# Performance work log

Measured on AMD Instinct MI355X. Metric: run time of the kernel, lower is better.

Reference implementation:

```python
import jax, jax.numpy as jnp
import numpy as np

N = 8192
IN_CH = 256
HID = 256
NEG_INF = -1000000000.0


def setup_inputs() -> dict:
    key = jax.random.key(0)
    ks = jax.random.split(key, 7)
    inlayer = jax.random.normal(ks[0], (N, IN_CH), dtype=jnp.float32)
    adj_mat = jax.random.randint(ks[1], (N, N), 0, 2, dtype=jnp.int32)
    # Xavier-uniform style scales
    s0 = (6.0 / (IN_CH + HID)) ** 0.5
    s1 = (6.0 / (HID + 1)) ** 0.5
    W = jax.random.uniform(ks[2], (HID, IN_CH), jnp.float32, -s0, s0)   # conv1d.weight[:, :, 0]
    w1 = jax.random.uniform(ks[3], (1, HID), jnp.float32, -s1, s1)      # conv1d1.weight[:, :, 0]
    b1 = jax.random.uniform(ks[4], (1,), jnp.float32, -s1, s1)          # conv1d1.bias
    w2 = jax.random.uniform(ks[5], (1, HID), jnp.float32, -s1, s1)      # conv1d2.weight[:, :, 0]
    b2 = jax.random.uniform(ks[6], (1,), jnp.float32, -s1, s1)          # conv1d2.bias
    return {"inlayer": inlayer, "adj_mat": adj_mat, "W": W,
            "w1": w1, "b1": b1, "w2": w2, "b2": b2}


def reference(inlayer, adj_mat, W, w1, b1, w2, b2):
    # 1x1 conv == linear projection: in_fts [HID, N]
    in_fts = W @ inlayer.T
    f1 = (w1 @ in_fts).T + b1          # [N, 1]
    f2 = (w2 @ in_fts).T + b2          # [N, 1]
    logits = f1 + f2.T                 # [N, N] broadcast add
    bias_mat = jnp.where(adj_mat > 0, 0.0, NEG_INF).astype(logits.dtype)
    coefs = jax.nn.softmax(jax.nn.leaky_relu(logits) + bias_mat, axis=-1)
    vals = coefs @ inlayer             # [N, IN_CH]
    return vals
```

## Files before the change

kernel.cpp:

```cpp
#include <hip/hip_runtime.h>
#include <hip/hip_bf16.h>

typedef float f32x4 __attribute__((ext_vector_type(4)));
typedef __bf16 bf16x8 __attribute__((ext_vector_type(8)));

#define N 8192
#define CH 256
#define NJC 2
#define JCW (N / NJC)
#define JT 128
#define NT (JCW / JT)
#define BM 64

static constexpr size_t OFF_P1 = 0;
static constexpr size_t OFF_P2 = 32768;
static constexpr size_t OFF_T1 = 65536;
static constexpr size_t OFF_T2 = 66560;
static constexpr size_t OFF_F1 = 67584;
static constexpr size_t OFF_F2 = OFF_F1 + (size_t)N * 4;
static constexpr size_t OFF_XT = 262144;
static constexpr size_t OFF_SP = OFF_XT + (size_t)CH * N * 2;
static constexpr size_t OFF_PV = OFF_SP + (size_t)NJC * N * 4;

__global__ __launch_bounds__(256) void k1a(
    const float* __restrict__ W, const float* __restrict__ w1,
    const float* __restrict__ w2, float* __restrict__ p1, float* __restrict__ p2)
{
    int b = blockIdx.x, c = threadIdx.x;
    float a1 = 0.f, a2 = 0.f;
#pragma unroll
    for (int hh = 0; hh < 8; ++hh) {
        int h = b * 8 + hh;
        float wv = W[h * CH + c];
        a1 = __builtin_fmaf(w1[h], wv, a1);
        a2 = __builtin_fmaf(w2[h], wv, a2);
    }
    p1[b * CH + c] = a1;
    p2[b * CH + c] = a2;
}

__global__ __launch_bounds__(256) void k1b(
    const float* __restrict__ p1, const float* __restrict__ p2,
    float* __restrict__ t1, float* __restrict__ t2)
{
    int c = threadIdx.x;
    float a1 = 0.f, a2 = 0.f;
#pragma unroll 8
    for (int b = 0; b < 32; ++b) { a1 += p1[b * CH + c]; a2 += p2[b * CH + c]; }
    t1[c] = a1;
    t2[c] = a2;
}

__global__ __launch_bounds__(256) void ktf(
    const float* __restrict__ x, const float* __restrict__ t1,
    const float* __restrict__ t2, const float* __restrict__ b1,
    const float* __restrict__ b2, unsigned short* __restrict__ xtp,
    float* __restrict__ f1, float* __restrict__ f2)
{
    __shared__ unsigned short tile[32][264];
    int js32 = blockIdx.x;
    int jb = js32 * 32;
    int t = threadIdx.x;
    int lane = t & 63;
    int wv = t >> 6;
    const float4* t1v = (const float4*)t1;
    const float4* t2v = (const float4*)t2;
    float4 ta = t1v[lane], tb = t2v[lane];
    float bb1 = b1[0], bb2 = b2[0];
#pragma unroll
    for (int it = 0; it < 8; ++it) {
        int jr = it * 4 + wv;
        float4 v = *(const float4*)(x + (size_t)(jb + jr) * CH + lane * 4);
        __hip_bfloat16 h0 = __float2bfloat16(v.x);
        __hip_bfloat16 h1 = __float2bfloat16(v.y);
        __hip_bfloat16 h2 = __float2bfloat16(v.z);
        __hip_bfloat16 h3 = __float2bfloat16(v.w);
        tile[jr][lane * 4 + 0] = *(unsigned short*)&h0;
        tile[jr][lane * 4 + 1] = *(unsigned short*)&h1;
        tile[jr][lane * 4 + 2] = *(unsigned short*)&h2;
        tile[jr][lane * 4 + 3] = *(unsigned short*)&h3;
        float d1 = v.x * ta.x + v.y * ta.y + v.z * ta.z + v.w * ta.w;
        float d2 = v.x * tb.x + v.y * tb.y + v.z * tb.z + v.w * tb.w;
#pragma unroll
        for (int off = 32; off; off >>= 1) {
            d1 += __shfl_down(d1, off);
            d2 += __shfl_down(d2, off);
        }
        if (lane == 0) { f1[jb + jr] = d1 + bb1; f2[jb + jr] = d2 + bb2; }
    }
    __syncthreads();
    int r = lane & 15, q = lane >> 4;
#pragma unroll
    for (int pass = 0; pass < 4; ++pass) {
        int ct = pass * 4 + wv;
        unsigned short vs[8];
#pragma unroll
        for (int e = 0; e < 8; ++e) vs[e] = tile[q * 8 + e][ct * 16 + r];
        size_t u = ((size_t)ct * 256 + js32) * 64 + lane;
        *(ulonglong2*)(xtp + u * 8) = *(ulonglong2*)vs;
    }
}

#define BAR() { asm volatile("s_waitcnt lgkmcnt(0)" ::: "memory"); \
                __builtin_amdgcn_s_barrier(); }

__global__ __launch_bounds__(1024, 4) void k34_fused(
    const int* __restrict__ adj, const float* __restrict__ f1,
    const float* __restrict__ f2, const unsigned short* __restrict__ xtp,
    float* __restrict__ pv0, float* __restrict__ pvx, float* __restrict__ s_part)
{
    __shared__ __align__(16) unsigned short P[2][BM * JT];
    __shared__ __align__(16) float f2s[JCW];

    const int tid = threadIdx.x;
    const int lane = tid & 63;
    const int w = tid >> 6;
    const int r = lane & 15, q = lane >> 4;
    const int bid = blockIdx.x;
    const int jc = bid & 1;
    const int rb = (bid >> 1) * BM;
    const int jbase = jc * JCW;
    const bool cons = (w < 8);

    const int ptid = tid - 512;
    const int prow = (ptid >> 3) & 63;
    const int pjo = (ptid & 7) * 16;
    const int* aptr = adj + (size_t)(rb + prow) * N + jbase + pjo;
    const int s0i = (ptid & 7) * 2;
    const int wu0 = prow * 16 + (s0i ^ (prow & 7));
    const int wu1 = prow * 16 + ((s0i + 1) ^ (prow & 7));
    float f1r = 0.f;
    if (!cons) f1r = f1[rb + prow];

    const unsigned short* xb0 = xtp + (((size_t)(w * 2) * 256 + jc * (JCW / 32)) * 64 + lane) * 8;
    const unsigned short* xb1 = xtp + (((size_t)(w * 2 + 1) * 256 + jc * (JCW / 32)) * 64 + lane) * 8;

    f32x4 acc[4][2];
#pragma unroll
    for (int mt = 0; mt < 4; ++mt)
#pragma unroll
        for (int nt = 0; nt < 2; ++nt) acc[mt][nt] = (f32x4){0.f, 0.f, 0.f, 0.f};
    float s_acc = 0.f;

    int4 RA0, RA1, RA2, RA3, RB0, RB1, RB2, RB3;

#define LOAD_A(R0, R1, R2, R3, t)                                   \
    { const int4* p_ = (const int4*)(aptr + (size_t)(t) * JT);      \
      R0 = p_[0]; R1 = p_[1]; R2 = p_[2]; R3 = p_[3]; }
#define EXPW(R0, R1, R2, R3, buf, tt)                               \
    { float4 g0 = *(const float4*)(&f2s[(tt) * JT + pjo]);          \
      float4 g1 = *(const float4*)(&f2s[(tt) * JT + pjo + 4]);      \
      float4 g2 = *(const float4*)(&f2s[(tt) * JT + pjo + 8]);      \
      float4 g3 = *(const float4*)(&f2s[(tt) * JT + pjo + 12]);     \
      int av[16] = {R0.x, R0.y, R0.z, R0.w, R1.x, R1.y, R1.z, R1.w, \
                    R2.x, R2.y, R2.z, R2.w, R3.x, R3.y, R3.z, R3.w};\
      float gv[16] = {g0.x, g0.y, g0.z, g0.w, g1.x, g1.y, g1.z, g1.w,\
                      g2.x, g2.y, g2.z, g2.w, g3.x, g3.y, g3.z, g3.w};\
      bf16x8 pk0, pk1;                                              \
      _Pragma("unroll")                                             \
      for (int e = 0; e < 16; ++e) {                                \
          float t_ = f1r + gv[e];                                   \
          t_ = fmaxf(t_, 0.01f * t_);                               \
          float p_ = (av[e] > 0) ? __expf(t_) : 0.f;                \
          s_acc += p_;                                              \
          if (e < 8) pk0[e] = (__bf16)p_; else pk1[e - 8] = (__bf16)p_; \
      }                                                             \
      *reinterpret_cast<bf16x8*>(&P[buf][(size_t)wu0 * 8]) = pk0;   \
      *reinterpret_cast<bf16x8*>(&P[buf][(size_t)wu1 * 8]) = pk1; }
#define MFMA_TILE(tt, buf)                                          \
    { _Pragma("unroll")                                             \
      for (int kk = 0; kk < 4; ++kk) {                              \
          bf16x8 B0 = *(const bf16x8*)(xb0 + ((size_t)((tt) * 4 + kk) * 64) * 8); \
          bf16x8 B1 = *(const bf16x8*)(xb1 + ((size_t)((tt) * 4 + kk) * 64) * 8); \
          _Pragma("unroll")                                         \
          for (int mt = 0; mt < 4; ++mt) {                          \
              int u_ = (mt * 16 + r) * 16 + ((kk * 4 + q) ^ (r & 7)); \
              bf16x8 A = *(const bf16x8*)(&P[buf][(size_t)u_ * 8]); \
              acc[mt][0] = __builtin_amdgcn_mfma_f32_16x16x32_bf16(A, B0, acc[mt][0], 0, 0, 0); \
              acc[mt][1] = __builtin_amdgcn_mfma_f32_16x16x32_bf16(A, B1, acc[mt][1], 0, 0, 0); \
          }                                                         \
      } }

    *(float4*)(&f2s[tid * 4]) = *(const float4*)(f2 + jbase + tid * 4);

    if (!cons) {
        LOAD_A(RA0, RA1, RA2, RA3, 0);
        LOAD_A(RB0, RB1, RB2, RB3, 1);
    }
    __syncthreads();
    if (!cons) EXPW(RA0, RA1, RA2, RA3, 0, 0);
    BAR();

    for (int t = 0; t < NT; t += 2) {
        if (cons) {
            MFMA_TILE(t, 0);
        } else {
            if (t + 2 < NT) LOAD_A(RA0, RA1, RA2, RA3, t + 2);
            EXPW(RB0, RB1, RB2, RB3, 1, t + 1);
        }
        BAR();
        if (cons) {
            MFMA_TILE(t + 1, 1);
        } else {
            if (t + 3 < NT) LOAD_A(RB0, RB1, RB2, RB3, t + 3);
            if (t + 2 < NT) EXPW(RA0, RA1, RA2, RA3, 0, t + 2);
        }
        BAR();
    }

    if (!cons) {
        s_acc += __shfl_xor(s_acc, 1);
        s_acc += __shfl_xor(s_acc, 2);
        s_acc += __shfl_xor(s_acc, 4);
        if ((lane & 7) == 0) s_part[jc * N + rb + prow] = s_acc;
    } else {
        float* dst = (jc == 0) ? pv0 : pvx;
#pragma unroll
        for (int mt = 0; mt < 4; ++mt)
#pragma unroll
            for (int nt = 0; nt < 2; ++nt)
#pragma unroll
                for (int reg = 0; reg < 4; ++reg) {
                    int row = rb + mt * 16 + q * 4 + reg;
                    int col = w * 32 + nt * 16 + r;
                    dst[(size_t)row * CH + col] = acc[mt][nt][reg];
                }
    }
#undef LOAD_A
#undef EXPW
#undef MFMA_TILE
}

__global__ __launch_bounds__(256) void k5_reduce(
    const float* __restrict__ pvx, const float* __restrict__ s_part,
    float* __restrict__ out)
{
    int g = blockIdx.x * 256 + threadIdx.x;
    int row = g >> 6;
    float s = s_part[row] + s_part[N + row];
    float inv = (s != 0.f) ? 1.0f / s : 0.f;
    float4* out4 = (float4*)out;
    const float4* p1 = (const float4*)pvx;
    float4 v = out4[g];
    float4 a = p1[g];
    v.x = (v.x + a.x) * inv;
    v.y = (v.y + a.y) * inv;
    v.z = (v.z + a.z) * inv;
    v.w = (v.w + a.w) * inv;
    out4[g] = v;
}

extern "C" void kernel_launch(void* const* d_in, const int* in_sizes, int n_in,
                              void* d_out, int out_size, void* d_ws, size_t ws_size,
                              hipStream_t stream)
{
    const float* inlayer = (const float*)d_in[0];
    const int*   adj     = (const int*)d_in[1];
    const float* W       = (const float*)d_in[2];
    const float* w1      = (const float*)d_in[3];
    const float* b1      = (const float*)d_in[4];
    const float* w2      = (const float*)d_in[5];
    const float* b2      = (const float*)d_in[6];
    float* out = (float*)d_out;

    char* ws = (char*)d_ws;
    float* p1 = (float*)(ws + OFF_P1);
    float* p2 = (float*)(ws + OFF_P2);
    float* t1 = (float*)(ws + OFF_T1);
    float* t2 = (float*)(ws + OFF_T2);
    float* f1 = (float*)(ws + OFF_F1);
    float* f2 = (float*)(ws + OFF_F2);
    unsigned short* xtp = (unsigned short*)(ws + OFF_XT);
    float* s_part = (float*)(ws + OFF_SP);
    float* pvx = (float*)(ws + OFF_PV);

    k1a<<<dim3(32), dim3(256), 0, stream>>>(W, w1, w2, p1, p2);
    k1b<<<dim3(1), dim3(256), 0, stream>>>(p1, p2, t1, t2);
    ktf<<<dim3(N / 32), dim3(256), 0, stream>>>(
        inlayer, t1, t2, b1, b2, xtp, f1, f2);
    k34_fused<<<dim3((N / BM) * NJC), dim3(1024), 0, stream>>>(
        adj, f1, f2, xtp, out, pvx, s_part);
    k5_reduce<<<dim3(N * CH / 4 / 256), dim3(256), 0, stream>>>(pvx, s_part, out);
}
```

Measured before the change: 101.8 us.

## Split columns into four chunks with 512-thread blocks and wider per-wave MFMA tiles

Moves the fused attention kernel from a 2-way to a 4-way split of the key dimension and halves the j-tile width. Blocks shrink to 512 threads (4 consumer and 4 producer waves). Each consumer wave now covers 64 output columns with 4x4 accumulators, and its MFMA section is raised in priority with s_setprio. This gives twice as many smaller blocks to improve occupancy and load balance, at the cost of two extra partial-output buffers that the reduce kernel must read and sum.

```diff
diff --git a/kernel.cpp b/kernel.cpp
--- a/kernel.cpp
+++ b/kernel.cpp
@@ -6,9 +6,9 @@
 
 #define N 8192
 #define CH 256
-#define NJC 2
+#define NJC 4
 #define JCW (N / NJC)
-#define JT 128
+#define JT 64
 #define NT (JCW / JT)
 #define BM 64
 
@@ -104,7 +104,7 @@
 #define BAR() { asm volatile("s_waitcnt lgkmcnt(0)" ::: "memory"); \
                 __builtin_amdgcn_s_barrier(); }
 
-__global__ __launch_bounds__(1024, 4) void k34_fused(
+__global__ __launch_bounds__(512, 4) void k34_fused(
     const int* __restrict__ adj, const float* __restrict__ f1,
     const float* __restrict__ f2, const unsigned short* __restrict__ xtp,
     float* __restrict__ pv0, float* __restrict__ pvx, float* __restrict__ s_part)
@@ -117,29 +117,26 @@
     const int w = tid >> 6;
     const int r = lane & 15, q = lane >> 4;
     const int bid = blockIdx.x;
-    const int jc = bid & 1;
-    const int rb = (bid >> 1) * BM;
+    const int jc = bid & 3;
+    const int rb = (bid >> 2) * BM;
     const int jbase = jc * JCW;
-    const bool cons = (w < 8);
-
-    const int ptid = tid - 512;
-    const int prow = (ptid >> 3) & 63;
-    const int pjo = (ptid & 7) * 16;
+    const bool cons = (w < 4);
+
+    const int ptid = (tid - 256) & 255;
+    const int prow = ptid >> 2;
+    const int pjo = (ptid & 3) * 16;
     const int* aptr = adj + (size_t)(rb + prow) * N + jbase + pjo;
-    const int s0i = (ptid & 7) * 2;
-    const int wu0 = prow * 16 + (s0i ^ (prow & 7));
-    const int wu1 = prow * 16 + ((s0i + 1) ^ (prow & 7));
+    const int s0i = (ptid & 3) * 2;
+    const int wu0 = prow * 8 + (s0i ^ (prow & 7));
+    const int wu1 = prow * 8 + ((s0i + 1) ^ (prow & 7));
     float f1r = 0.f;
     if (!cons) f1r = f1[rb + prow];
 
-    const unsigned short* xb0 = xtp + (((size_t)(w * 2) * 256 + jc * (JCW / 32)) * 64 + lane) * 8;
-    const unsigned short* xb1 = xtp + (((size_t)(w * 2 + 1) * 256 + jc * (JCW / 32)) * 64 + lane) * 8;
-
-    f32x4 acc[4][2];
+    f32x4 acc[4][4];
 #pragma unroll
     for (int mt = 0; mt < 4; ++mt)
 #pragma unroll
-        for (int nt = 0; nt < 2; ++nt) acc[mt][nt] = (f32x4){0.f, 0.f, 0.f, 0.f};
+        for (int i = 0; i < 4; ++i) acc[mt][i] = (f32x4){0.f, 0.f, 0.f, 0.f};
     float s_acc = 0.f;
 
     int4 RA0, RA1, RA2, RA3, RB0, RB1, RB2, RB3;
@@ -168,25 +165,31 @@
       *reinterpret_cast<bf16x8*>(&P[buf][(size_t)wu0 * 8]) = pk0;   \
       *reinterpret_cast<bf16x8*>(&P[buf][(size_t)wu1 * 8]) = pk1; }
 #define MFMA_TILE(tt, buf)                                          \
-    { _Pragma("unroll")                                             \
-      for (int kk = 0; kk < 4; ++kk) {                              \
-          bf16x8 B0 = *(const bf16x8*)(xb0 + ((size_t)((tt) * 4 + kk) * 64) * 8); \
-          bf16x8 B1 = *(const bf16x8*)(xb1 + ((size_t)((tt) * 4 + kk) * 64) * 8); \
+    { __builtin_amdgcn_s_setprio(1);                                \
+      _Pragma("unroll")                                             \
+      for (int kk = 0; kk < 2; ++kk) {                              \
+          bf16x8 Bv[4];                                             \
+          _Pragma("unroll")                                         \
+          for (int i = 0; i < 4; ++i) {                             \
+              size_t u_ = ((size_t)(w * 4 + i) * 256 + jc * 64 + (tt) * 2 + kk) * 64 + lane; \
+              Bv[i] = *(const bf16x8*)(xtp + u_ * 8);               \
+          }                                                         \
           _Pragma("unroll")                                         \
           for (int mt = 0; mt < 4; ++mt) {                          \
-              int u_ = (mt * 16 + r) * 16 + ((kk * 4 + q) ^ (r & 7)); \
-              bf16x8 A = *(const bf16x8*)(&P[buf][(size_t)u_ * 8]); \
-              acc[mt][0] = __builtin_amdgcn_mfma_f32_16x16x32_bf16(A, B0, acc[mt][0], 0, 0, 0); \
-              acc[mt][1] = __builtin_amdgcn_mfma_f32_16x16x32_bf16(A, B1, acc[mt][1], 0, 0, 0); \
+              int ua = (mt * 16 + r) * 8 + ((kk * 4 + q) ^ (r & 7));\
+              bf16x8 A = *(const bf16x8*)(&P[buf][(size_t)ua * 8]); \
+              _Pragma("unroll")                                     \
+              for (int i = 0; i < 4; ++i)                           \
+                  acc[mt][i] = __builtin_amdgcn_mfma_f32_16x16x32_bf16(A, Bv[i], acc[mt][i], 0, 0, 0); \
           }                                                         \
-      } }
-
-    *(float4*)(&f2s[tid * 4]) = *(const float4*)(f2 + jbase + tid * 4);
+      }                                                             \
+      __builtin_amdgcn_s_setprio(0); }
 
     if (!cons) {
         LOAD_A(RA0, RA1, RA2, RA3, 0);
         LOAD_A(RB0, RB1, RB2, RB3, 1);
     }
+    *(float4*)(&f2s[tid * 4]) = *(const float4*)(f2 + jbase + tid * 4);
     __syncthreads();
     if (!cons) EXPW(RA0, RA1, RA2, RA3, 0, 0);
     BAR();
@@ -211,19 +214,18 @@
     if (!cons) {
         s_acc += __shfl_xor(s_acc, 1);
         s_acc += __shfl_xor(s_acc, 2);
-        s_acc += __shfl_xor(s_acc, 4);
-        if ((lane & 7) == 0) s_part[jc * N + rb + prow] = s_acc;
+        if ((lane & 3) == 0) s_part[jc * N + rb + prow] = s_acc;
     } else {
-        float* dst = (jc == 0) ? pv0 : pvx;
+        float* dst = (jc == 0) ? pv0 : (pvx + (size_t)(jc - 1) * N * CH);
 #pragma unroll
         for (int mt = 0; mt < 4; ++mt)
 #pragma unroll
-            for (int nt = 0; nt < 2; ++nt)
+            for (int i = 0; i < 4; ++i)
 #pragma unroll
                 for (int reg = 0; reg < 4; ++reg) {
                     int row = rb + mt * 16 + q * 4 + reg;
-                    int col = w * 32 + nt * 16 + r;
-                    dst[(size_t)row * CH + col] = acc[mt][nt][reg];
+                    int col = (w * 4 + i) * 16 + r;
+                    dst[(size_t)row * CH + col] = acc[mt][i][reg];
                 }
     }
 #undef LOAD_A
@@ -237,16 +239,18 @@
 {
     int g = blockIdx.x * 256 + threadIdx.x;
     int row = g >> 6;
-    float s = s_part[row] + s_part[N + row];
+    float s = s_part[row] + s_part[N + row] + s_part[2 * N + row] + s_part[3 * N + row];
     float inv = (s != 0.f) ? 1.0f / s : 0.f;
     float4* out4 = (float4*)out;
     const float4* p1 = (const float4*)pvx;
+    const float4* p2 = p1 + (size_t)N * CH / 4;
+    const float4* p3 = p2 + (size_t)N * CH / 4;
     float4 v = out4[g];
-    float4 a = p1[g];
-    v.x = (v.x + a.x) * inv;
-    v.y = (v.y + a.y) * inv;
-    v.z = (v.z + a.z) * inv;
-    v.w = (v.w + a.w) * inv;
+    float4 a = p1[g], b = p2[g], c = p3[g];
+    v.x = (v.x + a.x + b.x + c.x) * inv;
+    v.y = (v.y + a.y + b.y + c.y) * inv;
+    v.z = (v.z + a.z + b.z + c.z) * inv;
+    v.w = (v.w + a.w + b.w + c.w) * inv;
     out4[g] = v;
 }
 
@@ -278,7 +282,7 @@
     k1b<<<dim3(1), dim3(256), 0, stream>>>(p1, p2, t1, t2);
     ktf<<<dim3(N / 32), dim3(256), 0, stream>>>(
         inlayer, t1, t2, b1, b2, xtp, f1, f2);
-    k34_fused<<<dim3((N / BM) * NJC), dim3(1024), 0, stream>>>(
+    k34_fused<<<dim3((N / BM) * NJC), dim3(512), 0, stream>>>(
         adj, f1, f2, xtp, out, pvx, s_part);
     k5_reduce<<<dim3(N * CH / 4 / 256), dim3(256), 0, stream>>>(pvx, s_part, out);
 }
```

After: 162.4 us. +59.6%, slower.

## Replace producer/consumer LDS pipeline with register-resident per-wave exp+MFMA over 8 column splits

Applied to the files above, without the earlier changes.

The attention kernel drops the warp-specialized producer/consumer scheme that staged bf16 probabilities through shared memory with barriers. Each wave now computes exp weights for 32 rows directly into MFMA A-operand registers and multiplies them against the pre-packed bf16 features loaded straight from global memory, accumulating all 256 output columns in registers. The column dimension is split 8 ways instead of 2 to keep enough blocks in flight, so the reduce kernel now sums 8 partial outputs and 8 partial row sums. This removes LDS traffic and barriers but raises register pressure, re-reads the feature matrix per wave from L2, and adds extra partial-output write and read traffic.

```diff
diff --git a/kernel.cpp b/kernel.cpp
--- a/kernel.cpp
+++ b/kernel.cpp
@@ -6,11 +6,9 @@
 
 #define N 8192
 #define CH 256
-#define NJC 2
+#define NJC 8
 #define JCW (N / NJC)
-#define JT 128
-#define NT (JCW / JT)
-#define BM 64
+#define NS (JCW / 32)
 
 static constexpr size_t OFF_P1 = 0;
 static constexpr size_t OFF_P2 = 32768;
@@ -101,134 +99,97 @@
     }
 }
 
-#define BAR() { asm volatile("s_waitcnt lgkmcnt(0)" ::: "memory"); \
-                __builtin_amdgcn_s_barrier(); }
-
-__global__ __launch_bounds__(1024, 4) void k34_fused(
+__global__ __launch_bounds__(256, 2) void k34_fused(
     const int* __restrict__ adj, const float* __restrict__ f1,
     const float* __restrict__ f2, const unsigned short* __restrict__ xtp,
     float* __restrict__ pv0, float* __restrict__ pvx, float* __restrict__ s_part)
 {
-    __shared__ __align__(16) unsigned short P[2][BM * JT];
-    __shared__ __align__(16) float f2s[JCW];
-
     const int tid = threadIdx.x;
     const int lane = tid & 63;
     const int w = tid >> 6;
     const int r = lane & 15, q = lane >> 4;
     const int bid = blockIdx.x;
-    const int jc = bid & 1;
-    const int rb = (bid >> 1) * BM;
+    const int jc = bid & 7;
+    const int rb = (bid >> 3) * 128 + w * 32;
     const int jbase = jc * JCW;
-    const bool cons = (w < 8);
-
-    const int ptid = tid - 512;
-    const int prow = (ptid >> 3) & 63;
-    const int pjo = (ptid & 7) * 16;
-    const int* aptr = adj + (size_t)(rb + prow) * N + jbase + pjo;
-    const int s0i = (ptid & 7) * 2;
-    const int wu0 = prow * 16 + (s0i ^ (prow & 7));
-    const int wu1 = prow * 16 + ((s0i + 1) ^ (prow & 7));
-    float f1r = 0.f;
-    if (!cons) f1r = f1[rb + prow];
-
-    const unsigned short* xb0 = xtp + (((size_t)(w * 2) * 256 + jc * (JCW / 32)) * 64 + lane) * 8;
-    const unsigned short* xb1 = xtp + (((size_t)(w * 2 + 1) * 256 + jc * (JCW / 32)) * 64 + lane) * 8;
-
-    f32x4 acc[4][2];
-#pragma unroll
-    for (int mt = 0; mt < 4; ++mt)
-#pragma unroll
-        for (int nt = 0; nt < 2; ++nt) acc[mt][nt] = (f32x4){0.f, 0.f, 0.f, 0.f};
-    float s_acc = 0.f;
-
-    int4 RA0, RA1, RA2, RA3, RB0, RB1, RB2, RB3;
-
-#define LOAD_A(R0, R1, R2, R3, t)                                   \
-    { const int4* p_ = (const int4*)(aptr + (size_t)(t) * JT);      \
-      R0 = p_[0]; R1 = p_[1]; R2 = p_[2]; R3 = p_[3]; }
-#define EXPW(R0, R1, R2, R3, buf, tt)                               \
-    { float4 g0 = *(const float4*)(&f2s[(tt) * JT + pjo]);          \
-      float4 g1 = *(const float4*)(&f2s[(tt) * JT + pjo + 4]);      \
-      float4 g2 = *(const float4*)(&f2s[(tt) * JT + pjo + 8]);      \
-      float4 g3 = *(const float4*)(&f2s[(tt) * JT + pjo + 12]);     \
-      int av[16] = {R0.x, R0.y, R0.z, R0.w, R1.x, R1.y, R1.z, R1.w, \
-                    R2.x, R2.y, R2.z, R2.w, R3.x, R3.y, R3.z, R3.w};\
-      float gv[16] = {g0.x, g0.y, g0.z, g0.w, g1.x, g1.y, g1.z, g1.w,\
-                      g2.x, g2.y, g2.z, g2.w, g3.x, g3.y, g3.z, g3.w};\
-      bf16x8 pk0, pk1;                                              \
+
+    const float f1r0 = f1[rb + r];
+    const float f1r1 = f1[rb + 16 + r];
+    const int* arow0 = adj + (size_t)(rb + r) * N + jbase + q * 8;
+    const int* arow1 = arow0 + (size_t)16 * N;
+    const float* f2p = f2 + jbase + q * 8;
+
+    f32x4 acc0[16], acc1[16];
+#pragma unroll
+    for (int ct = 0; ct < 16; ++ct) {
+        acc0[ct] = (f32x4){0.f, 0.f, 0.f, 0.f};
+        acc1[ct] = (f32x4){0.f, 0.f, 0.f, 0.f};
+    }
+    float s0 = 0.f, s1 = 0.f;
+
+    int4 A0a, A0b, A1a, A1b;
+    int4 B0a, B0b, B1a, B1b;
+
+#define LOAD(Xa, Xb, Ya, Yb, t)                                     \
+    { const int4* p0_ = (const int4*)(arow0 + (size_t)(t) * 32);    \
+      const int4* p1_ = (const int4*)(arow1 + (size_t)(t) * 32);    \
+      Xa = p0_[0]; Xb = p0_[1]; Ya = p1_[0]; Yb = p1_[1]; }
+#define COMPUTE(Xa, Xb, Ya, Yb, t)                                  \
+    { float4 g0 = *(const float4*)(f2p + (size_t)(t) * 32);         \
+      float4 g1 = *(const float4*)(f2p + (size_t)(t) * 32 + 4);     \
+      int av0[8] = {Xa.x, Xa.y, Xa.z, Xa.w, Xb.x, Xb.y, Xb.z, Xb.w};\
+      int av1[8] = {Ya.x, Ya.y, Ya.z, Ya.w, Yb.x, Yb.y, Yb.z, Yb.w};\
+      float gv[8] = {g0.x, g0.y, g0.z, g0.w, g1.x, g1.y, g1.z, g1.w};\
+      bf16x8 pka, pkb;                                              \
       _Pragma("unroll")                                             \
-      for (int e = 0; e < 16; ++e) {                                \
-          float t_ = f1r + gv[e];                                   \
-          t_ = fmaxf(t_, 0.01f * t_);                               \
-          float p_ = (av[e] > 0) ? __expf(t_) : 0.f;                \
-          s_acc += p_;                                              \
-          if (e < 8) pk0[e] = (__bf16)p_; else pk1[e - 8] = (__bf16)p_; \
+      for (int e = 0; e < 8; ++e) {                                 \
+          float ta_ = f1r0 + gv[e];                                 \
+          ta_ = fmaxf(ta_, 0.01f * ta_);                            \
+          float pa_ = (av0[e] > 0) ? __expf(ta_) : 0.f;             \
+          s0 += pa_;                                                \
+          pka[e] = (__bf16)pa_;                                     \
+          float tb_ = f1r1 + gv[e];                                 \
+          tb_ = fmaxf(tb_, 0.01f * tb_);                            \
+          float pb_ = (av1[e] > 0) ? __expf(tb_) : 0.f;             \
+          s1 += pb_;                                                \
+          pkb[e] = (__bf16)pb_;                                     \
       }                                                             \
-      *reinterpret_cast<bf16x8*>(&P[buf][(size_t)wu0 * 8]) = pk0;   \
-      *reinterpret_cast<bf16x8*>(&P[buf][(size_t)wu1 * 8]) = pk1; }
-#define MFMA_TILE(tt, buf)                                          \
-    { _Pragma("unroll")                                             \
-      for (int kk = 0; kk < 4; ++kk) {                              \
-          bf16x8 B0 = *(const bf16x8*)(xb0 + ((size_t)((tt) * 4 + kk) * 64) * 8); \
-          bf16x8 B1 = *(const bf16x8*)(xb1 + ((size_t)((tt) * 4 + kk) * 64) * 8); \
-          _Pragma("unroll")                                         \
-          for (int mt = 0; mt < 4; ++mt) {                          \
-              int u_ = (mt * 16 + r) * 16 + ((kk * 4 + q) ^ (r & 7)); \
-              bf16x8 A = *(const bf16x8*)(&P[buf][(size_t)u_ * 8]); \
-              acc[mt][0] = __builtin_amdgcn_mfma_f32_16x16x32_bf16(A, B0, acc[mt][0], 0, 0, 0); \
-              acc[mt][1] = __builtin_amdgcn_mfma_f32_16x16x32_bf16(A, B1, acc[mt][1], 0, 0, 0); \
-          }                                                         \
+      _Pragma("unroll")                                             \
+      for (int ct = 0; ct < 16; ++ct) {                             \
+          size_t u_ = ((size_t)ct * 256 + jc * NS + (t)) * 64 + lane; \
+          bf16x8 Bv = *(const bf16x8*)(xtp + u_ * 8);               \
+          acc0[ct] = __builtin_amdgcn_mfma_f32_16x16x32_bf16(pka, Bv, acc0[ct], 0, 0, 0); \
+          acc1[ct] = __builtin_amdgcn_mfma_f32_16x16x32_bf16(pkb, Bv, acc1[ct], 0, 0, 0); \
       } }
 
-    *(float4*)(&f2s[tid * 4]) = *(const float4*)(f2 + jbase + tid * 4);
-
-    if (!cons) {
-        LOAD_A(RA0, RA1, RA2, RA3, 0);
-        LOAD_A(RB0, RB1, RB2, RB3, 1);
-    }
-    __syncthreads();
-    if (!cons) EXPW(RA0, RA1, RA2, RA3, 0, 0);
-    BAR();
-
-    for (int t = 0; t < NT; t += 2) {
-        if (cons) {
-            MFMA_TILE(t, 0);
-        } else {
-            if (t + 2 < NT) LOAD_A(RA0, RA1, RA2, RA3, t + 2);
-            EXPW(RB0, RB1, RB2, RB3, 1, t + 1);
+    LOAD(A0a, A0b, A1a, A1b, 0);
+    LOAD(B0a, B0b, B1a, B1b, 1);
+
+    for (int t = 0; t < NS; t += 2) {
+        COMPUTE(A0a, A0b, A1a, A1b, t);
+        if (t + 2 < NS) LOAD(A0a, A0b, A1a, A1b, t + 2);
+        COMPUTE(B0a, B0b, B1a, B1b, t + 1);
+        if (t + 3 < NS) LOAD(B0a, B0b, B1a, B1b, t + 3);
+    }
+
+    s0 += __shfl_xor(s0, 16); s0 += __shfl_xor(s0, 32);
+    s1 += __shfl_xor(s1, 16); s1 += __shfl_xor(s1, 32);
+    if (lane < 16) {
+        s_part[(size_t)jc * N + rb + lane] = s0;
+        s_part[(size_t)jc * N + rb + 16 + lane] = s1;
+    }
+
+    float* dst = (jc == 0) ? pv0 : (pvx + (size_t)(jc - 1) * N * CH);
+#pragma unroll
+    for (int ct = 0; ct < 16; ++ct)
+#pragma unroll
+        for (int reg = 0; reg < 4; ++reg) {
+            int row0 = rb + q * 4 + reg;
+            dst[(size_t)row0 * CH + ct * 16 + r] = acc0[ct][reg];
+            dst[(size_t)(row0 + 16) * CH + ct * 16 + r] = acc1[ct][reg];
         }
-        BAR();
-        if (cons) {
-            MFMA_TILE(t + 1, 1);
-        } else {
-            if (t + 3 < NT) LOAD_A(RB0, RB1, RB2, RB3, t + 3);
-            if (t + 2 < NT) EXPW(RA0, RA1, RA2, RA3, 0, t + 2);
-        }
-        BAR();
-    }
-
-    if (!cons) {
-        s_acc += __shfl_xor(s_acc, 1);
-        s_acc += __shfl_xor(s_acc, 2);
-        s_acc += __shfl_xor(s_acc, 4);
-        if ((lane & 7) == 0) s_part[jc * N + rb + prow] = s_acc;
-    } else {
-        float* dst = (jc == 0) ? pv0 : pvx;
-#pragma unroll
-        for (int mt = 0; mt < 4; ++mt)
-#pragma unroll
-            for (int nt = 0; nt < 2; ++nt)
-#pragma unroll
-                for (int reg = 0; reg < 4; ++reg) {
-                    int row = rb + mt * 16 + q * 4 + reg;
-                    int col = w * 32 + nt * 16 + r;
-                    dst[(size_t)row * CH + col] = acc[mt][nt][reg];
-                }
-    }
-#undef LOAD_A
-#undef EXPW
-#undef MFMA_TILE
+#undef LOAD
+#undef COMPUTE
 }
 
 __global__ __launch_bounds__(256) void k5_reduce(
@@ -237,16 +198,18 @@
 {
     int g = blockIdx.x * 256 + threadIdx.x;
     int row = g >> 6;
-    float s = s_part[row] + s_part[N + row];
+    float s = 0.f;
+#pragma unroll
+    for (int k = 0; k < NJC; ++k) s += s_part[(size_t)k * N + row];
     float inv = (s != 0.f) ? 1.0f / s : 0.f;
     float4* out4 = (float4*)out;
-    const float4* p1 = (const float4*)pvx;
     float4 v = out4[g];
-    float4 a = p1[g];
-    v.x = (v.x + a.x) * inv;
-    v.y = (v.y + a.y) * inv;
-    v.z = (v.z + a.z) * inv;
-    v.w = (v.w + a.w) * inv;
+#pragma unroll
+    for (int k = 0; k < NJC - 1; ++k) {
+        float4 a = ((const float4*)(pvx + (size_t)k * N * CH))[g];
+        v.x += a.x; v.y += a.y; v.z += a.z; v.w += a.w;
+    }
+    v.x *= inv; v.y *= inv; v.z *= inv; v.w *= inv;
     out4[g] = v;
 }
 
@@ -278,7 +241,7 @@
     k1b<<<dim3(1), dim3(256), 0, stream>>>(p1, p2, t1, t2);
     ktf<<<dim3(N / 32), dim3(256), 0, stream>>>(
         inlayer, t1, t2, b1, b2, xtp, f1, f2);
-    k34_fused<<<dim3((N / BM) * NJC), dim3(1024), 0, stream>>>(
+    k34_fused<<<dim3((N / 128) * NJC), dim3(256), 0, stream>>>(
         adj, f1, f2, xtp, out, pvx, s_part);
     k5_reduce<<<dim3(N * CH / 4 / 256), dim3(256), 0, stream>>>(pvx, s_part, out);
 }
```

Result: slower. 176.1 us (+73.0%).

## Factor exp of leaky-relu into precomputed per-node exponentials and split columns four ways

Applied to the files above, without the earlier changes.

Replaces the per-element exp(leaky_relu(f1+f2)) with a product of exponentials precomputed per node: exp(f1)*exp(f2) when the logit is positive, otherwise exp(0.01 f1)*exp(0.01 f2). The hot loop then does multiplies and a select instead of a transcendental. The column split also goes from 2 to 4 chunks with a higher occupancy hint, and the final reduction sums more partials. The risk is that products of large exponentials overflow in fp32, since there is no max subtraction. It also adds more partial-output traffic and LDS per block.

```diff
diff --git a/kernel.cpp b/kernel.cpp
--- a/kernel.cpp
+++ b/kernel.cpp
@@ -6,7 +6,7 @@
 
 #define N 8192
 #define CH 256
-#define NJC 2
+#define NJC 4
 #define JCW (N / NJC)
 #define JT 128
 #define NT (JCW / JT)
@@ -16,8 +16,10 @@
 static constexpr size_t OFF_P2 = 32768;
 static constexpr size_t OFF_T1 = 65536;
 static constexpr size_t OFF_T2 = 66560;
-static constexpr size_t OFF_F1 = 67584;
-static constexpr size_t OFF_F2 = OFF_F1 + (size_t)N * 4;
+static constexpr size_t OFF_E1 = 67584;
+static constexpr size_t OFF_G1 = OFF_E1 + (size_t)N * 4;
+static constexpr size_t OFF_E2 = OFF_G1 + (size_t)N * 4;
+static constexpr size_t OFF_G2 = OFF_E2 + (size_t)N * 4;
 static constexpr size_t OFF_XT = 262144;
 static constexpr size_t OFF_SP = OFF_XT + (size_t)CH * N * 2;
 static constexpr size_t OFF_PV = OFF_SP + (size_t)NJC * N * 4;
@@ -55,7 +57,8 @@
     const float* __restrict__ x, const float* __restrict__ t1,
     const float* __restrict__ t2, const float* __restrict__ b1,
     const float* __restrict__ b2, unsigned short* __restrict__ xtp,
-    float* __restrict__ f1, float* __restrict__ f2)
+    float* __restrict__ E1g, float* __restrict__ G1g,
+    float* __restrict__ E2g, float* __restrict__ G2g)
 {
     __shared__ unsigned short tile[32][264];
     int js32 = blockIdx.x;
@@ -86,7 +89,13 @@
             d1 += __shfl_down(d1, off);
             d2 += __shfl_down(d2, off);
         }
-        if (lane == 0) { f1[jb + jr] = d1 + bb1; f2[jb + jr] = d2 + bb2; }
+        if (lane == 0) {
+            float f1 = d1 + bb1, f2 = d2 + bb2;
+            E1g[jb + jr] = __expf(f1);
+            G1g[jb + jr] = __expf(0.01f * f1);
+            E2g[jb + jr] = __expf(f2);
+            G2g[jb + jr] = __expf(0.01f * f2);
+        }
     }
     __syncthreads();
     int r = lane & 15, q = lane >> 4;
@@ -104,21 +113,23 @@
 #define BAR() { asm volatile("s_waitcnt lgkmcnt(0)" ::: "memory"); \
                 __builtin_amdgcn_s_barrier(); }
 
-__global__ __launch_bounds__(1024, 4) void k34_fused(
-    const int* __restrict__ adj, const float* __restrict__ f1,
-    const float* __restrict__ f2, const unsigned short* __restrict__ xtp,
+__global__ __launch_bounds__(1024, 8) void k34_fused(
+    const int* __restrict__ adj, const float* __restrict__ E1g,
+    const float* __restrict__ G1g, const float* __restrict__ E2g,
+    const float* __restrict__ G2g, const unsigned short* __restrict__ xtp,
     float* __restrict__ pv0, float* __restrict__ pvx, float* __restrict__ s_part)
 {
     __shared__ __align__(16) unsigned short P[2][BM * JT];
-    __shared__ __align__(16) float f2s[JCW];
+    __shared__ __align__(16) float e2s[JCW];
+    __shared__ __align__(16) float g2s[JCW];
 
     const int tid = threadIdx.x;
     const int lane = tid & 63;
     const int w = tid >> 6;
     const int r = lane & 15, q = lane >> 4;
     const int bid = blockIdx.x;
-    const int jc = bid & 1;
-    const int rb = (bid >> 1) * BM;
+    const int jc = bid & 3;
+    const int rb = (bid >> 2) * BM;
     const int jbase = jc * JCW;
     const bool cons = (w < 8);
 
@@ -129,8 +140,8 @@
     const int s0i = (ptid & 7) * 2;
     const int wu0 = prow * 16 + (s0i ^ (prow & 7));
     const int wu1 = prow * 16 + ((s0i + 1) ^ (prow & 7));
-    float f1r = 0.f;
-    if (!cons) f1r = f1[rb + prow];
+    float E1r = 0.f, G1r = 0.f;
+    if (!cons) { E1r = E1g[rb + prow]; G1r = G1g[rb + prow]; }
 
     const unsigned short* xb0 = xtp + (((size_t)(w * 2) * 256 + jc * (JCW / 32)) * 64 + lane) * 8;
     const unsigned short* xb1 = xtp + (((size_t)(w * 2 + 1) * 256 + jc * (JCW / 32)) * 64 + lane) * 8;
@@ -148,20 +159,27 @@
     { const int4* p_ = (const int4*)(aptr + (size_t)(t) * JT);      \
       R0 = p_[0]; R1 = p_[1]; R2 = p_[2]; R3 = p_[3]; }
 #define EXPW(R0, R1, R2, R3, buf, tt)                               \
-    { float4 g0 = *(const float4*)(&f2s[(tt) * JT + pjo]);          \
-      float4 g1 = *(const float4*)(&f2s[(tt) * JT + pjo + 4]);      \
-      float4 g2 = *(const float4*)(&f2s[(tt) * JT + pjo + 8]);      \
-      float4 g3 = *(const float4*)(&f2s[(tt) * JT + pjo + 12]);     \
+    { float4 g0 = *(const float4*)(&e2s[(tt) * JT + pjo]);          \
+      float4 g1 = *(const float4*)(&e2s[(tt) * JT + pjo + 4]);      \
+      float4 g2 = *(const float4*)(&e2s[(tt) * JT + pjo + 8]);      \
+      float4 g3 = *(const float4*)(&e2s[(tt) * JT + pjo + 12]);     \
+      float4 h0 = *(const float4*)(&g2s[(tt) * JT + pjo]);          \
+      float4 h1 = *(const float4*)(&g2s[(tt) * JT + pjo + 4]);      \
+      float4 h2 = *(const float4*)(&g2s[(tt) * JT + pjo + 8]);      \
+      float4 h3 = *(const float4*)(&g2s[(tt) * JT + pjo + 12]);     \
       int av[16] = {R0.x, R0.y, R0.z, R0.w, R1.x, R1.y, R1.z, R1.w, \
                     R2.x, R2.y, R2.z, R2.w, R3.x, R3.y, R3.z, R3.w};\
       float gv[16] = {g0.x, g0.y, g0.z, g0.w, g1.x, g1.y, g1.z, g1.w,\
                       g2.x, g2.y, g2.z, g2.w, g3.x, g3.y, g3.z, g3.w};\
+      float hv[16] = {h0.x, h0.y, h0.z, h0.w, h1.x, h1.y, h1.z, h1.w,\
+                      h2.x, h2.y, h2.z, h2.w, h3.x, h3.y, h3.z, h3.w};\
       bf16x8 pk0, pk1;                                              \
       _Pragma("unroll")                                             \
       for (int e = 0; e < 16; ++e) {                                \
-          float t_ = f1r + gv[e];                                   \
-          t_ = fmaxf(t_, 0.01f * t_);                               \
-          float p_ = (av[e] > 0) ? __expf(t_) : 0.f;                \
+          float te = E1r * gv[e];                                   \
+          float tf = G1r * hv[e];                                   \
+          float p_ = (te > 1.0f) ? te : tf;                         \
+          p_ = (av[e] > 0) ? p_ : 0.f;                              \
           s_acc += p_;                                              \
           if (e < 8) pk0[e] = (__bf16)p_; else pk1[e - 8] = (__bf16)p_; \
       }                                                             \
@@ -181,7 +199,8 @@
           }                                                         \
       } }
 
-    *(float4*)(&f2s[tid * 4]) = *(const float4*)(f2 + jbase + tid * 4);
+    *(float2*)(&e2s[tid * 2]) = *(const float2*)(E2g + jbase + tid * 2);
+    *(float2*)(&g2s[tid * 2]) = *(const float2*)(G2g + jbase + tid * 2);
 
     if (!cons) {
         LOAD_A(RA0, RA1, RA2, RA3, 0);
@@ -214,7 +233,7 @@
         s_acc += __shfl_xor(s_acc, 4);
         if ((lane & 7) == 0) s_part[jc * N + rb + prow] = s_acc;
     } else {
-        float* dst = (jc == 0) ? pv0 : pvx;
+        float* dst = (jc == 0) ? pv0 : (pvx + (size_t)(jc - 1) * N * CH);
 #pragma unroll
         for (int mt = 0; mt < 4; ++mt)
 #pragma unroll
@@ -237,16 +256,18 @@
 {
     int g = blockIdx.x * 256 + threadIdx.x;
     int row = g >> 6;
-    float s = s_part[row] + s_part[N + row];
+    float s = s_part[row] + s_part[N + row] + s_part[2 * N + row] + s_part[3 * N + row];
     float inv = (s != 0.f) ? 1.0f / s : 0.f;
     float4* out4 = (float4*)out;
     const float4* p1 = (const float4*)pvx;
+    const float4* p2 = p1 + (size_t)N * CH / 4;
+    const float4* p3 = p2 + (size_t)N * CH / 4;
     float4 v = out4[g];
-    float4 a = p1[g];
-    v.x = (v.x + a.x) * inv;
-    v.y = (v.y + a.y) * inv;
-    v.z = (v.z + a.z) * inv;
-    v.w = (v.w + a.w) * inv;
+    float4 a = p1[g], b = p2[g], c = p3[g];
+    v.x = (v.x + a.x + b.x + c.x) * inv;
+    v.y = (v.y + a.y + b.y + c.y) * inv;
+    v.z = (v.z + a.z + b.z + c.z) * inv;
+    v.w = (v.w + a.w + b.w + c.w) * inv;
     out4[g] = v;
 }
 
@@ -268,8 +289,10 @@
     float* p2 = (float*)(ws + OFF_P2);
     float* t1 = (float*)(ws + OFF_T1);
     float* t2 = (float*)(ws + OFF_T2);
-    float* f1 = (float*)(ws + OFF_F1);
-    float* f2 = (float*)(ws + OFF_F2);
+    float* E1g = (float*)(ws + OFF_E1);
+    float* G1g = (float*)(ws + OFF_G1);
+    float* E2g = (float*)(ws + OFF_E2);
+    float* G2g = (float*)(ws + OFF_G2);
     unsigned short* xtp = (unsigned short*)(ws + OFF_XT);
     float* s_part = (float*)(ws + OFF_SP);
     float* pvx = (float*)(ws + OFF_PV);
@@ -277,8 +300,8 @@
     k1a<<<dim3(32), dim3(256), 0, stream>>>(W, w1, w2, p1, p2);
     k1b<<<dim3(1), dim3(256), 0, stream>>>(p1, p2, t1, t2);
     ktf<<<dim3(N / 32), dim3(256), 0, stream>>>(
-        inlayer, t1, t2, b1, b2, xtp, f1, f2);
+        inlayer, t1, t2, b1, b2, xtp, E1g, G1g, E2g, G2g);
     k34_fused<<<dim3((N / BM) * NJC), dim3(1024), 0, stream>>>(
-        adj, f1, f2, xtp, out, pvx, s_part);
+        adj, E1g, G1g, E2g, G2g, xtp, out, pvx, s_part);
     k5_reduce<<<dim3(N * CH / 4 / 256), dim3(256), 0, stream>>>(pvx, s_part, out);
 }
```

New measurement: 358.7 us. 253% more time.
